# Optimization experiments

Measured on AMD Instinct MI355X. Metric: run time of the kernel, lower is better.

Reference implementation:

```python
import jax, jax.numpy as jnp
import numpy as np

N, TX, TZ, DX, DZ, DATT, DOUT = 8, 2048, 2048, 1024, 1024, 1024, 1024


def setup_inputs() -> dict:
    key = jax.random.key(0)
    ks = jax.random.split(key, 8)
    s = 0.02
    x = jax.random.normal(ks[0], (N, TX, DX), dtype=jnp.float32)
    z = jax.random.normal(ks[1], (N, TZ, DZ), dtype=jnp.float32)
    Wq = jax.random.normal(ks[2], (DX, DATT), dtype=jnp.float32) * s
    bq = jnp.zeros((DATT,), dtype=jnp.float32)
    Wk = jax.random.normal(ks[3], (DZ, DATT), dtype=jnp.float32) * s
    bk = jnp.zeros((DATT,), dtype=jnp.float32)
    Wv = jax.random.normal(ks[4], (DZ, DOUT), dtype=jnp.float32) * s
    bv = jnp.zeros((DOUT,), dtype=jnp.float32)
    # fixed boolean mask [Tx, Tz]; causal lower-triangular so no row is fully masked
    mask = jnp.tril(jnp.ones((TX, TZ), dtype=bool))
    return {"x": x, "z": z, "Wq": Wq, "bq": bq, "Wk": Wk, "bk": bk,
            "Wv": Wv, "bv": bv, "mask": mask}


def reference(x, z, Wq, bq, Wk, bk, Wv, bv, mask):
    Datt = Wq.shape[1]
    Q = x @ Wq + bq                      # [N, Tx, Datt]
    K = z @ Wk + bk                      # [N, Tz, Datt]
    V = z @ Wv + bv                      # [N, Tz, Dout]
    S = jnp.einsum('bxd,bzd->bxz', Q, K)  # [N, Tx, Tz]
    S = jnp.where(mask[None, :, :], S, -jnp.inf)
    A = jax.nn.softmax(S / jnp.sqrt(jnp.float32(Datt)), axis=-1)
    y = jnp.einsum('bxz,bzo->bxo', A, V)  # [N, Tx, Dout]
    return y
```

## Files before the change

kernel.cpp:

```cpp
#include <hip/hip_runtime.h>

typedef _Float16 f16;
typedef _Float16 f16x8 __attribute__((ext_vector_type(8)));
typedef _Float16 f16x4 __attribute__((ext_vector_type(4)));
typedef float    f32x4 __attribute__((ext_vector_type(4)));

constexpr int NB   = 8;
constexpr int T    = 2048;
constexpr int D    = 1024;
constexpr int NTRI = 136;

__device__ __forceinline__ void load_lds16(const f16* g, f16* l) {
    __builtin_amdgcn_global_load_lds(
        (const __attribute__((address_space(1))) void*)g,
        (__attribute__((address_space(3))) void*)l, 16, 0, 0);
}

__global__ __launch_bounds__(256) void cast_transpose_w(
    const float* __restrict__ W0, const float* __restrict__ W1,
    const float* __restrict__ W2, f16* __restrict__ Wt)
{
    __shared__ f16 tile[32][33];
    const int which = blockIdx.z;
    const float* W = which == 0 ? W0 : (which == 1 ? W1 : W2);
    f16* dst = Wt + (size_t)which * D * D;
    const int c0 = blockIdx.x * 32, r0 = blockIdx.y * 32;
    const int tx = threadIdx.x & 31, ty = threadIdx.x >> 5;
    #pragma unroll
    for (int i = 0; i < 32; i += 8)
        tile[ty + i][tx] = (f16)W[(size_t)(r0 + ty + i) * D + c0 + tx];
    __syncthreads();
    #pragma unroll
    for (int i = 0; i < 32; i += 8)
        dst[(size_t)(c0 + ty + i) * D + r0 + tx] = tile[tx][ty + i];
}

__global__ __launch_bounds__(256) void cast_xz(
    const float* __restrict__ x, const float* __restrict__ z,
    f16* __restrict__ xh, f16* __restrict__ zh)
{
    const float* src = blockIdx.y ? z : x;
    f16* dst = blockIdx.y ? zh : xh;
    const size_t i = ((size_t)blockIdx.x * 256 + threadIdx.x) * 4;
    const float4 v = *(const float4*)(src + i);
    f16x4 u = { (f16)v.x, (f16)v.y, (f16)v.z, (f16)v.w };
    *(f16x4*)(dst + i) = u;
}

template<int MODE>
__global__ __launch_bounds__(256) void gemm_nt(
    const f16* __restrict__ Ag_, const f16* __restrict__ Bg_,
    void* __restrict__ Cg_, const float* __restrict__ bias)
{
    __shared__ f16 As[128 * 32];
    __shared__ f16 Bs[128 * 32];

    int bx, by;
    const int bz = blockIdx.z;
    if (MODE == 1) {
        const int idx = blockIdx.x;
        by = (int)((sqrtf(8.0f * idx + 1.0f) - 1.0f) * 0.5f);
        while ((by + 1) * (by + 2) / 2 <= idx) ++by;
        while (by * (by + 1) / 2 > idx) --by;
        bx = idx - by * (by + 1) / 2;
    } else { bx = blockIdx.x; by = blockIdx.y; }

    const size_t bm0 = (size_t)by * 128, bn0 = (size_t)bx * 128;
    const f16* Abase; const f16* Bbase;
    int lda, ldb, K;
    if (MODE == 0 || MODE == 3) {
        Abase = Ag_ + bm0 * D;                       lda = D;
        Bbase = Bg_ + bn0 * D;                       ldb = D; K = D;
    } else if (MODE == 1) {
        Abase = Ag_ + (size_t)bz * T * D + bm0 * D;  lda = D;
        Bbase = Bg_ + (size_t)bz * T * D + bn0 * D;  ldb = D; K = D;
    } else {
        Abase = Ag_ + ((size_t)bz * NTRI + (size_t)by * (by + 1) / 2) * 16384;
        lda = 128;
        Bbase = Bg_ + (size_t)bz * D * T + bn0 * T;  ldb = T;
        K = (by + 1) * 128;
    }

    const int t    = threadIdx.x;
    const int lane = t & 63, wave = t >> 6;
    const int wr   = (wave >> 1) * 64, wc = (wave & 1) * 64;
    const int fr   = lane & 15, fo = (lane >> 4) * 8;
    const int srow = t >> 2;
    const int scol = (t & 3) * 8;
    const int wub  = (t & 192) * 8;

    f32x4 acc[4][4] = {};

    for (int k0 = 0; k0 < K; k0 += 32) {
        const f16* Ak;
        if (MODE == 2) Ak = Abase + (size_t)(k0 >> 7) * 16384 + (k0 & 127);
        else           Ak = Abase + k0;
        #pragma unroll
        for (int it = 0; it < 2; ++it)
            load_lds16(Ak + (size_t)(it * 64 + srow) * lda + scol,
                       As + it * 2048 + wub);
        #pragma unroll
        for (int it = 0; it < 2; ++it)
            load_lds16(Bbase + k0 + (size_t)(it * 64 + srow) * ldb + scol,
                       Bs + it * 2048 + wub);
        __syncthreads();

        f16x8 av[4], bv[4];
        #pragma unroll
        for (int i = 0; i < 4; ++i)
            av[i] = *(const f16x8*)&As[(wr + i * 16 + fr) * 32 + fo];
        #pragma unroll
        for (int j = 0; j < 4; ++j)
            bv[j] = *(const f16x8*)&Bs[(wc + j * 16 + fr) * 32 + fo];
        #pragma unroll
        for (int i = 0; i < 4; ++i)
            #pragma unroll
            for (int j = 0; j < 4; ++j)
                acc[i][j] = __builtin_amdgcn_mfma_f32_16x16x32_f16(av[i], bv[j], acc[i][j], 0, 0, 0);
        __syncthreads();
    }

    const int cr = (lane >> 4) * 4, cc = lane & 15;
    if (MODE == 0) {
        f16* Cp = (f16*)Cg_;
        #pragma unroll
        for (int j = 0; j < 4; ++j) {
            const int col = (int)bn0 + wc + j * 16 + cc;
            const float bb = bias[col];
            #pragma unroll
            for (int i = 0; i < 4; ++i)
                #pragma unroll
                for (int g = 0; g < 4; ++g)
                    Cp[(bm0 + wr + i * 16 + cr + g) * D + col] = (f16)(acc[i][j][g] + bb);
        }
    } else if (MODE == 3) {
        f16* Vt = (f16*)Cg_;
        const int b  = (int)(bm0 >> 11);
        const int r0 = (int)(bm0 & 2047);
        #pragma unroll
        for (int j = 0; j < 4; ++j) {
            const int col = (int)bn0 + wc + j * 16 + cc;
            const float bb = bias[col];
            #pragma unroll
            for (int i = 0; i < 4; ++i) {
                f16x4 pk = { (f16)(acc[i][j][0] + bb), (f16)(acc[i][j][1] + bb),
                             (f16)(acc[i][j][2] + bb), (f16)(acc[i][j][3] + bb) };
                *(f16x4*)&Vt[(size_t)b * D * T + (size_t)col * T + r0 + wr + i * 16 + cr] = pk;
            }
        }
    } else if (MODE == 1) {
        f16* Cp = (f16*)Cg_ + ((size_t)bz * NTRI + (size_t)by * (by + 1) / 2 + bx) * 16384;
        #pragma unroll
        for (int i = 0; i < 4; ++i)
            #pragma unroll
            for (int j = 0; j < 4; ++j)
                #pragma unroll
                for (int g = 0; g < 4; ++g) {
                    const int lr = wr + i * 16 + cr + g, lc = wc + j * 16 + cc;
                    const int gr = (int)bm0 + lr, gc = (int)bn0 + lc;
                    Cp[lr * 128 + lc] = (gc > gr) ? (f16)(-30000.0f)
                                                  : (f16)(acc[i][j][g] * 0.03125f);
                }
    } else {
        float* Cp = (float*)Cg_ + (size_t)bz * T * D;
        #pragma unroll
        for (int i = 0; i < 4; ++i)
            #pragma unroll
            for (int j = 0; j < 4; ++j)
                #pragma unroll
                for (int g = 0; g < 4; ++g)
                    Cp[(bm0 + wr + i * 16 + cr + g) * D + bn0 + wc + j * 16 + cc] = acc[i][j][g];
    }
}

__global__ __launch_bounds__(256) void softmax_rows(f16* __restrict__ SA)
{
    const int r = blockIdx.x, b = blockIdx.y;
    const int ib  = r >> 7;
    const int len = (ib + 1) << 7;
    f16* base = SA + ((size_t)b * NTRI + (size_t)ib * (ib + 1) / 2) * 16384
                   + (size_t)(r & 127) * 128;
    const int t = threadIdx.x;

    float vals[8];
    float m = -3.4e38f;
    #pragma unroll
    for (int i = 0; i < 8; ++i) {
        const int j = t + i * 256;
        const float v = (j < len)
            ? (float)base[(size_t)(j >> 7) * 16384 + (j & 127)] : -3.4e38f;
        vals[i] = v;
        m = fmaxf(m, v);
    }
    #pragma unroll
    for (int o = 32; o > 0; o >>= 1) m = fmaxf(m, __shfl_xor(m, o, 64));
    __shared__ float red[4];
    if ((t & 63) == 0) red[t >> 6] = m;
    __syncthreads();
    m = fmaxf(fmaxf(red[0], red[1]), fmaxf(red[2], red[3]));
    __syncthreads();

    float s = 0.f;
    #pragma unroll
    for (int i = 0; i < 8; ++i) {
        const float e = __expf(vals[i] - m);
        vals[i] = e;
        s += e;
    }
    #pragma unroll
    for (int o = 32; o > 0; o >>= 1) s += __shfl_xor(s, o, 64);
    if ((t & 63) == 0) red[t >> 6] = s;
    __syncthreads();
    s = (red[0] + red[1]) + (red[2] + red[3]);
    const float rinv = 1.0f / s;

    #pragma unroll
    for (int i = 0; i < 8; ++i) {
        const int j = t + i * 256;
        if (j < len) base[(size_t)(j >> 7) * 16384 + (j & 127)] = (f16)(vals[i] * rinv);
    }
}

extern "C" void kernel_launch(void* const* d_in, const int* in_sizes, int n_in,
                              void* d_out, int out_size, void* d_ws, size_t ws_size,
                              hipStream_t stream)
{
    const float* x  = (const float*)d_in[0];
    const float* z  = (const float*)d_in[1];
    const float* Wq = (const float*)d_in[2];
    const float* bq = (const float*)d_in[3];
    const float* Wk = (const float*)d_in[4];
    const float* bk = (const float*)d_in[5];
    const float* Wv = (const float*)d_in[6];
    const float* bv = (const float*)d_in[7];
    float* out = (float*)d_out;

    char* ws = (char*)d_ws;
    f16* Wt = (f16*)(ws);
    f16* xh = (f16*)(ws + 6291456ull);
    f16* zh = (f16*)(ws + 39845888ull);
    f16* Qh = (f16*)(ws + 73400320ull);
    f16* Kh = (f16*)(ws + 106954752ull);
    f16* Vt = (f16*)(ws + 140509184ull);
    f16* SA = (f16*)(ws + 174063616ull);

    cast_transpose_w<<<dim3(32, 32, 3), 256, 0, stream>>>(Wq, Wk, Wv, Wt);
    cast_xz<<<dim3(16384, 2, 1), 256, 0, stream>>>(x, z, xh, zh);
    gemm_nt<0><<<dim3(8, 128, 1), 256, 0, stream>>>(xh, Wt,           Qh, bq);
    gemm_nt<0><<<dim3(8, 128, 1), 256, 0, stream>>>(zh, Wt + 1048576, Kh, bk);
    gemm_nt<3><<<dim3(8, 128, 1), 256, 0, stream>>>(zh, Wt + 2097152, Vt, bv);
    gemm_nt<1><<<dim3(136, 1, 8), 256, 0, stream>>>(Qh, Kh, SA, nullptr);
    softmax_rows<<<dim3(2048, 8, 1), 256, 0, stream>>>(SA);
    gemm_nt<2><<<dim3(8, 16, 8), 256, 0, stream>>>(SA, Vt, out, nullptr);
}
```

Before: 534.8 us.

## Fuse softmax into score and PV GEMMs, merge K/V projection, widen K-step

Removes the separate softmax kernel. The QK^T GEMM epilogue now writes exp(scaled score) directly, with no max subtraction, and accumulates row sums via atomics. The PV GEMM epilogue divides by the row sum. K and V projections are merged into one launch over concatenated weights, and the GEMM main loop loads two 32-wide K slices per barrier to halve synchronisations. It also reverses block order for the triangular PV GEMM so longer rows start first. Skipping the max subtraction relies on small score magnitudes, which carries an overflow risk for general inputs, and atomics add nondeterminism.

Result: faster. 500.2 us (-6.5%).

```diff
diff --git a/kernel.cpp b/kernel.cpp
--- a/kernel.cpp
+++ b/kernel.cpp
@@ -50,10 +50,12 @@
 template<int MODE>
 __global__ __launch_bounds__(256) void gemm_nt(
     const f16* __restrict__ Ag_, const f16* __restrict__ Bg_,
-    void* __restrict__ Cg_, const float* __restrict__ bias)
-{
-    __shared__ f16 As[128 * 32];
-    __shared__ f16 Bs[128 * 32];
+    void* __restrict__ Cg_, void* __restrict__ Cg2_,
+    const float* __restrict__ bias, const float* __restrict__ bias2,
+    float* __restrict__ rsum)
+{
+    __shared__ f16 As[2 * 128 * 32];
+    __shared__ f16 Bs[2 * 128 * 32];
 
     int bx, by;
     const int bz = blockIdx.z;
@@ -63,12 +65,16 @@
         while ((by + 1) * (by + 2) / 2 <= idx) ++by;
         while (by * (by + 1) / 2 > idx) --by;
         bx = idx - by * (by + 1) / 2;
-    } else { bx = blockIdx.x; by = blockIdx.y; }
+    } else if (MODE == 2) {
+        bx = blockIdx.x; by = 15 - blockIdx.y;
+    } else {
+        bx = blockIdx.x; by = blockIdx.y;
+    }
 
     const size_t bm0 = (size_t)by * 128, bn0 = (size_t)bx * 128;
     const f16* Abase; const f16* Bbase;
     int lda, ldb, K;
-    if (MODE == 0 || MODE == 3) {
+    if (MODE == 0 || MODE == 4) {
         Abase = Ag_ + bm0 * D;                       lda = D;
         Bbase = Bg_ + bn0 * D;                       ldb = D; K = D;
     } else if (MODE == 1) {
@@ -91,32 +97,39 @@
 
     f32x4 acc[4][4] = {};
 
-    for (int k0 = 0; k0 < K; k0 += 32) {
-        const f16* Ak;
-        if (MODE == 2) Ak = Abase + (size_t)(k0 >> 7) * 16384 + (k0 & 127);
-        else           Ak = Abase + k0;
-        #pragma unroll
-        for (int it = 0; it < 2; ++it)
-            load_lds16(Ak + (size_t)(it * 64 + srow) * lda + scol,
-                       As + it * 2048 + wub);
-        #pragma unroll
-        for (int it = 0; it < 2; ++it)
-            load_lds16(Bbase + k0 + (size_t)(it * 64 + srow) * ldb + scol,
-                       Bs + it * 2048 + wub);
+    for (int k0 = 0; k0 < K; k0 += 64) {
+        #pragma unroll
+        for (int p = 0; p < 2; ++p) {
+            const int k = k0 + p * 32;
+            const f16* Ak;
+            if (MODE == 2) Ak = Abase + (size_t)(k >> 7) * 16384 + (k & 127);
+            else           Ak = Abase + k;
+            #pragma unroll
+            for (int it = 0; it < 2; ++it)
+                load_lds16(Ak + (size_t)(it * 64 + srow) * lda + scol,
+                           As + p * 4096 + it * 2048 + wub);
+            #pragma unroll
+            for (int it = 0; it < 2; ++it)
+                load_lds16(Bbase + k + (size_t)(it * 64 + srow) * ldb + scol,
+                           Bs + p * 4096 + it * 2048 + wub);
+        }
         __syncthreads();
 
-        f16x8 av[4], bv[4];
-        #pragma unroll
-        for (int i = 0; i < 4; ++i)
-            av[i] = *(const f16x8*)&As[(wr + i * 16 + fr) * 32 + fo];
-        #pragma unroll
-        for (int j = 0; j < 4; ++j)
-            bv[j] = *(const f16x8*)&Bs[(wc + j * 16 + fr) * 32 + fo];
-        #pragma unroll
-        for (int i = 0; i < 4; ++i)
+        #pragma unroll
+        for (int p = 0; p < 2; ++p) {
+            f16x8 av[4], bv[4];
+            #pragma unroll
+            for (int i = 0; i < 4; ++i)
+                av[i] = *(const f16x8*)&As[p * 4096 + (wr + i * 16 + fr) * 32 + fo];
             #pragma unroll
             for (int j = 0; j < 4; ++j)
-                acc[i][j] = __builtin_amdgcn_mfma_f32_16x16x32_f16(av[i], bv[j], acc[i][j], 0, 0, 0);
+                bv[j] = *(const f16x8*)&Bs[p * 4096 + (wc + j * 16 + fr) * 32 + fo];
+            #pragma unroll
+            for (int i = 0; i < 4; ++i)
+                #pragma unroll
+                for (int j = 0; j < 4; ++j)
+                    acc[i][j] = __builtin_amdgcn_mfma_f32_16x16x32_f16(av[i], bv[j], acc[i][j], 0, 0, 0);
+        }
         __syncthreads();
     }
 
@@ -133,23 +146,39 @@
                 for (int g = 0; g < 4; ++g)
                     Cp[(bm0 + wr + i * 16 + cr + g) * D + col] = (f16)(acc[i][j][g] + bb);
         }
-    } else if (MODE == 3) {
-        f16* Vt = (f16*)Cg_;
-        const int b  = (int)(bm0 >> 11);
-        const int r0 = (int)(bm0 & 2047);
-        #pragma unroll
-        for (int j = 0; j < 4; ++j) {
-            const int col = (int)bn0 + wc + j * 16 + cc;
-            const float bb = bias[col];
-            #pragma unroll
-            for (int i = 0; i < 4; ++i) {
-                f16x4 pk = { (f16)(acc[i][j][0] + bb), (f16)(acc[i][j][1] + bb),
-                             (f16)(acc[i][j][2] + bb), (f16)(acc[i][j][3] + bb) };
-                *(f16x4*)&Vt[(size_t)b * D * T + (size_t)col * T + r0 + wr + i * 16 + cr] = pk;
+    } else if (MODE == 4) {
+        if (bx < 8) {
+            f16* Cp = (f16*)Cg_;
+            #pragma unroll
+            for (int j = 0; j < 4; ++j) {
+                const int col = (int)bn0 + wc + j * 16 + cc;
+                const float bb = bias[col];
+                #pragma unroll
+                for (int i = 0; i < 4; ++i)
+                    #pragma unroll
+                    for (int g = 0; g < 4; ++g)
+                        Cp[(bm0 + wr + i * 16 + cr + g) * D + col] = (f16)(acc[i][j][g] + bb);
+            }
+        } else {
+            f16* Vt = (f16*)Cg2_;
+            const int b  = (int)(bm0 >> 11);
+            const int r0 = (int)(bm0 & 2047);
+            #pragma unroll
+            for (int j = 0; j < 4; ++j) {
+                const int colv = (int)bn0 - 1024 + wc + j * 16 + cc;
+                const float bb = bias2[colv];
+                #pragma unroll
+                for (int i = 0; i < 4; ++i) {
+                    f16x4 pk = { (f16)(acc[i][j][0] + bb), (f16)(acc[i][j][1] + bb),
+                                 (f16)(acc[i][j][2] + bb), (f16)(acc[i][j][3] + bb) };
+                    *(f16x4*)&Vt[(size_t)b * D * T + (size_t)colv * T + r0 + wr + i * 16 + cr] = pk;
+                }
             }
         }
     } else if (MODE == 1) {
         f16* Cp = (f16*)Cg_ + ((size_t)bz * NTRI + (size_t)by * (by + 1) / 2 + bx) * 16384;
+        float* rs = rsum + (size_t)bz * T + bm0;
+        float rowsum[4][4] = {};
         #pragma unroll
         for (int i = 0; i < 4; ++i)
             #pragma unroll
@@ -157,67 +186,37 @@
                 #pragma unroll
                 for (int g = 0; g < 4; ++g) {
                     const int lr = wr + i * 16 + cr + g, lc = wc + j * 16 + cc;
-                    const int gr = (int)bm0 + lr, gc = (int)bn0 + lc;
-                    Cp[lr * 128 + lc] = (gc > gr) ? (f16)(-30000.0f)
-                                                  : (f16)(acc[i][j][g] * 0.03125f);
+                    const int r = (int)bm0 + lr, c = (int)bn0 + lc;
+                    const float p = (c > r) ? 0.0f : __expf(acc[i][j][g] * 0.03125f);
+                    Cp[lr * 128 + lc] = (f16)p;
+                    rowsum[i][g] += p;
                 }
+        #pragma unroll
+        for (int i = 0; i < 4; ++i)
+            #pragma unroll
+            for (int g = 0; g < 4; ++g) {
+                float s = rowsum[i][g];
+                s += __shfl_xor(s, 1, 64);
+                s += __shfl_xor(s, 2, 64);
+                s += __shfl_xor(s, 4, 64);
+                s += __shfl_xor(s, 8, 64);
+                if (cc == 0) atomicAdd(&rs[wr + i * 16 + cr + g], s);
+            }
     } else {
         float* Cp = (float*)Cg_ + (size_t)bz * T * D;
-        #pragma unroll
-        for (int i = 0; i < 4; ++i)
+        const float* rs = rsum + (size_t)bz * T;
+        #pragma unroll
+        for (int i = 0; i < 4; ++i) {
+            const int r4 = (int)bm0 + wr + i * 16 + cr;
+            float rinv[4];
+            #pragma unroll
+            for (int g = 0; g < 4; ++g) rinv[g] = 1.0f / rs[r4 + g];
             #pragma unroll
             for (int j = 0; j < 4; ++j)
                 #pragma unroll
                 for (int g = 0; g < 4; ++g)
-                    Cp[(bm0 + wr + i * 16 + cr + g) * D + bn0 + wc + j * 16 + cc] = acc[i][j][g];
-    }
-}
-
-__global__ __launch_bounds__(256) void softmax_rows(f16* __restrict__ SA)
-{
-    const int r = blockIdx.x, b = blockIdx.y;
-    const int ib  = r >> 7;
-    const int len = (ib + 1) << 7;
-    f16* base = SA + ((size_t)b * NTRI + (size_t)ib * (ib + 1) / 2) * 16384
-                   + (size_t)(r & 127) * 128;
-    const int t = threadIdx.x;
-
-    float vals[8];
-    float m = -3.4e38f;
-    #pragma unroll
-    for (int i = 0; i < 8; ++i) {
-        const int j = t + i * 256;
-        const float v = (j < len)
-            ? (float)base[(size_t)(j >> 7) * 16384 + (j & 127)] : -3.4e38f;
-        vals[i] = v;
-        m = fmaxf(m, v);
-    }
-    #pragma unroll
-    for (int o = 32; o > 0; o >>= 1) m = fmaxf(m, __shfl_xor(m, o, 64));
-    __shared__ float red[4];
-    if ((t & 63) == 0) red[t >> 6] = m;
-    __syncthreads();
-    m = fmaxf(fmaxf(red[0], red[1]), fmaxf(red[2], red[3]));
-    __syncthreads();
-
-    float s = 0.f;
-    #pragma unroll
-    for (int i = 0; i < 8; ++i) {
-        const float e = __expf(vals[i] - m);
-        vals[i] = e;
-        s += e;
-    }
-    #pragma unroll
-    for (int o = 32; o > 0; o >>= 1) s += __shfl_xor(s, o, 64);
-    if ((t & 63) == 0) red[t >> 6] = s;
-    __syncthreads();
-    s = (red[0] + red[1]) + (red[2] + red[3]);
-    const float rinv = 1.0f / s;
-
-    #pragma unroll
-    for (int i = 0; i < 8; ++i) {
-        const int j = t + i * 256;
-        if (j < len) base[(size_t)(j >> 7) * 16384 + (j & 127)] = (f16)(vals[i] * rinv);
+                    Cp[(size_t)(r4 + g) * D + bn0 + wc + j * 16 + cc] = acc[i][j][g] * rinv[g];
+        }
     }
 }
 
@@ -236,20 +235,20 @@
     float* out = (float*)d_out;
 
     char* ws = (char*)d_ws;
-    f16* Wt = (f16*)(ws);
-    f16* xh = (f16*)(ws + 6291456ull);
-    f16* zh = (f16*)(ws + 39845888ull);
-    f16* Qh = (f16*)(ws + 73400320ull);
-    f16* Kh = (f16*)(ws + 106954752ull);
-    f16* Vt = (f16*)(ws + 140509184ull);
-    f16* SA = (f16*)(ws + 174063616ull);
-
+    f16*   Wt   = (f16*)(ws);
+    f16*   xh   = (f16*)(ws + 6291456ull);
+    f16*   zh   = (f16*)(ws + 39845888ull);
+    f16*   Qh   = (f16*)(ws + 73400320ull);
+    f16*   Kh   = (f16*)(ws + 106954752ull);
+    f16*   Vt   = (f16*)(ws + 140509184ull);
+    f16*   SA   = (f16*)(ws + 174063616ull);
+    float* rsum = (float*)(ws + 209715200ull);
+
+    hipMemsetAsync(rsum, 0, (size_t)NB * T * sizeof(float), stream);
     cast_transpose_w<<<dim3(32, 32, 3), 256, 0, stream>>>(Wq, Wk, Wv, Wt);
     cast_xz<<<dim3(16384, 2, 1), 256, 0, stream>>>(x, z, xh, zh);
-    gemm_nt<0><<<dim3(8, 128, 1), 256, 0, stream>>>(xh, Wt,           Qh, bq);
-    gemm_nt<0><<<dim3(8, 128, 1), 256, 0, stream>>>(zh, Wt + 1048576, Kh, bk);
-    gemm_nt<3><<<dim3(8, 128, 1), 256, 0, stream>>>(zh, Wt + 2097152, Vt, bv);
-    gemm_nt<1><<<dim3(136, 1, 8), 256, 0, stream>>>(Qh, Kh, SA, nullptr);
-    softmax_rows<<<dim3(2048, 8, 1), 256, 0, stream>>>(SA);
-    gemm_nt<2><<<dim3(8, 16, 8), 256, 0, stream>>>(SA, Vt, out, nullptr);
-}
+    gemm_nt<0><<<dim3(8, 128, 1), 256, 0, stream>>>(xh, Wt, Qh, nullptr, bq, nullptr, nullptr);
+    gemm_nt<4><<<dim3(16, 128, 1), 256, 0, stream>>>(zh, Wt + 1048576, Kh, Vt, bk, bv, nullptr);
+    gemm_nt<1><<<dim3(136, 1, 8), 256, 0, stream>>>(Qh, Kh, SA, nullptr, nullptr, nullptr, rsum);
+    gemm_nt<2><<<dim3(8, 16, 8), 256, 0, stream>>>(SA, Vt, out, nullptr, nullptr, nullptr, rsum);
+}
```
